# Optimization experiments

Hardware: AMD Instinct MI355X
Metric: run time of the kernel (lower is better)

## Reference

```python
import jax, jax.numpy as jnp
import numpy as np

VNUMS = [4248, 4258, 5327, 3721, 5404, 2818]
B, C, H, W = 12, 64, 192, 192
DV, HID, BOX = 128, 256, 32


def _roi_patches(imgs, pros, imgbatch, box_len=BOX):
    # torchvision roi_align (aligned=False, sampling_ratio -> 1 sample per 1x1 bin):
    # bilinear sample at bin centers x1 + (j+0.5), y1 + (i+0.5)
    ar = jnp.arange(box_len, dtype=pros.dtype) + 0.5
    xs = pros[:, 0:1] - box_len / 2.0 + ar  # [G, box]
    ys = pros[:, 1:2] - box_len / 2.0 + ar  # [G, box]
    img_g = imgs[imgbatch]  # [G, C, H, W]

    def sample_one(img_chw, ys1, xs1):
        yy, xx = jnp.meshgrid(ys1, xs1, indexing="ij")  # [box, box]
        def per_c(ch):
            return jax.scipy.ndimage.map_coordinates(ch, [yy, xx], order=1, mode="nearest")
        return jax.vmap(per_c)(img_chw)  # [C, box, box]

    return jax.vmap(sample_one)(img_g, ys, xs)  # [G, C, box, box]


def setup_inputs() -> dict:
    key = jax.random.key(0)
    ks = jax.random.split(key, 6)
    G = 2 * B
    gtypes = np.array([(g // 2) % 6 if g % 2 == 0 else ((g // 2) + 3) % 6 for g in range(G)], dtype=np.int64)
    vnums_g = np.array([VNUMS[t] for t in gtypes])
    off = np.concatenate([[0], np.cumsum(vnums_g)])
    Nv = int(off[-1])  # 103104
    gar_of_vert = np.repeat(np.arange(G), vnums_g)
    idxs = []
    for t in range(6):
        gl = np.nonzero(gtypes == t)[0]
        idxs.append(np.concatenate([off[g] + np.arange(VNUMS[t]) for g in gl]).astype(np.int32))
    Din = DV + C
    pros = jax.random.uniform(ks[1], (G, 2), jnp.float32) * (H - 2.0 * BOX) + BOX
    inp = {
        "imgs": jax.random.normal(ks[0], (B, C, H, W), jnp.float32),
        "pros": pros,
        "x_verts": jax.random.normal(ks[2], (Nv, DV), jnp.float32),
        "W1": jax.random.normal(ks[3], (6, Din, HID), jnp.float32) / np.sqrt(Din).astype(np.float32),
        "W2": jax.random.normal(ks[4], (6, HID, HID), jnp.float32) / np.sqrt(HID).astype(np.float32),
        "W3": jax.random.normal(ks[5], (6, HID, 3), jnp.float32) / np.sqrt(HID).astype(np.float32),
        "imgbatch": jnp.asarray(np.arange(G) // 2, jnp.int32),
        "gar_of_vert": jnp.asarray(gar_of_vert, jnp.int32),
    }
    for t in range(6):
        inp[f"idx_t{t}"] = jnp.asarray(idxs[t])
    return inp


def reference(imgs, pros, x_verts, W1, W2, W3, imgbatch, gar_of_vert,
              idx_t0, idx_t1, idx_t2, idx_t3, idx_t4, idx_t5):
    # 1) roi_align patch extraction + pooled per-garment image feature
    patches = _roi_patches(imgs, pros, imgbatch)        # [G, C, 32, 32]
    garf = patches.mean(axis=(2, 3))                     # [G, C]
    # 2) per-vertex feature = [vertex feat | garment image feat]
    feat = jnp.concatenate([x_verts, garf[gar_of_vert]], axis=-1)  # [Nv, DV+C]
    # 3) MoE-style dispatch per garment type -> per-type expert MLP -> scatter-combine
    out = jnp.zeros((x_verts.shape[0], 3), feat.dtype)
    for t, idx in enumerate([idx_t0, idx_t1, idx_t2, idx_t3, idx_t4, idx_t5]):
        ft = feat[idx]                                   # gather (dispatch)
        h = jax.nn.relu(ft @ W1[t])
        h = jax.nn.relu(h @ W2[t])
        out = out.at[idx].set(h @ W3[t])                 # scatter (combine)
    return out
```

## Files before the change

### kernel.cpp

```cpp
#include <hip/hip_runtime.h>

typedef __attribute__((ext_vector_type(8))) short short8;
typedef __attribute__((ext_vector_type(4))) float float4_;

__device__ __forceinline__ unsigned short f2bf(float f) {
    unsigned u = __float_as_uint(f);
    u += 0x7FFFu + ((u >> 16) & 1u);
    return (unsigned short)(u >> 16);
}

#define GARF_BLOCKS 1536
#define PREP_BLOCKS 2784

__global__ void prep_garf(const float* __restrict__ imgs,
                          const float* __restrict__ pros,
                          const int* __restrict__ imgbatch,
                          const float* __restrict__ W1,
                          const float* __restrict__ W2,
                          const float* __restrict__ W3,
                          unsigned short* __restrict__ w1t,
                          unsigned short* __restrict__ w2t,
                          unsigned short* __restrict__ w3t,
                          float* __restrict__ garf) {
    const int tid = threadIdx.x;
    if (blockIdx.x < GARF_BLOCKS) {
        __shared__ float part[4];
        int pc = blockIdx.x;
        int g = pc >> 6, c = pc & 63;
        int b = imgbatch[g];
        float cx = pros[g * 2 + 0], cy = pros[g * 2 + 1];
        int i = tid >> 3;
        int j0 = (tid & 7) * 4;
        float y = cy - 16.0f + (float)i + 0.5f;
        float yf = floorf(y);
        float wy1 = y - yf, wy0 = 1.0f - wy1;
        int iy0 = min(max((int)yf, 0), 191), iy1 = min(max((int)yf + 1, 0), 191);
        const float* base = imgs + (size_t)(b * 64 + c) * 36864;
        const float* r0 = base + iy0 * 192;
        const float* r1 = base + iy1 * 192;
        float sum = 0.0f;
#pragma unroll
        for (int jj = 0; jj < 4; ++jj) {
            float x = cx - 16.0f + (float)(j0 + jj) + 0.5f;
            float xf = floorf(x);
            float wx1 = x - xf, wx0 = 1.0f - wx1;
            int ix0 = min(max((int)xf, 0), 191), ix1 = min(max((int)xf + 1, 0), 191);
            sum += wy0 * (wx0 * r0[ix0] + wx1 * r0[ix1]) +
                   wy1 * (wx0 * r1[ix0] + wx1 * r1[ix1]);
        }
        for (int s = 32; s >= 1; s >>= 1) sum += __shfl_xor(sum, s);
        if ((tid & 63) == 0) part[tid >> 6] = sum;
        __syncthreads();
        if (tid == 0)
            garf[g * 64 + c] = (part[0] + part[1] + part[2] + part[3]) * (1.0f / 1024.0f);
    } else {
        int id = (blockIdx.x - GARF_BLOCKS) * 256 + tid;
        if (id < 294912) {
            int t = id / 49152, r = id % 49152;
            int k = r >> 8, n = r & 255;
            w1t[t * 49152 + n * 192 + k] = f2bf(W1[id]);
        } else if (id < 688128) {
            int i2 = id - 294912;
            int t = i2 >> 16, r = i2 & 65535;
            int k = r >> 8, n = r & 255;
            w2t[t * 65536 + n * 256 + k] = f2bf(W2[i2]);
        } else if (id < 712704) {
            int i3 = id - 688128;
            int t = i3 >> 12, r = i3 & 4095;
            int n = r >> 8, k = r & 255;
            w3t[i3] = (n < 3) ? f2bf(W3[t * 768 + k * 3 + n]) : (unsigned short)0;
        }
    }
}

struct MoEArgs {
    const float* x_verts;
    const int* gar;
    const int* idx[6];
    const unsigned short* w1t;
    const unsigned short* w2t;
    const unsigned short* w3t;
    const float* garf;
    float* out;
    int cnt[6];
    int tile_end[6];
};

__global__ __launch_bounds__(256, 4) void moe_kernel(MoEArgs a) {
    __shared__ __align__(16) char smem[32768 + 512];
    char* sF = smem;
    int* sidx = (int*)(smem + 32768);
    int* sg = sidx + 64;

    const int tid = threadIdx.x;
    int bt = blockIdx.x;
    int t = 0;
    while (t < 5 && bt >= a.tile_end[t]) ++t;
    const int tile = bt - (t ? a.tile_end[t - 1] : 0);
    const int cnt = a.cnt[t];
    const int i0 = tile * 64;
    const int* idx = a.idx[t];

    if (tid < 64) {
        int m = i0 + tid;
        if (m > cnt - 1) m = cnt - 1;
        int vid = idx[m];
        sidx[tid] = vid;
        sg[tid] = a.gar[vid];
    }
    __syncthreads();

    for (int e = tid; e < 1536; e += 256) {
        int m = e / 24, u = e % 24;
        const float* src;
        if (u < 16) src = a.x_verts + (size_t)sidx[m] * 128 + u * 8;
        else        src = a.garf + sg[m] * 64 + (u - 16) * 8;
        float4 v0 = ((const float4*)src)[0];
        float4 v1 = ((const float4*)src)[1];
        short8 pk;
        pk[0] = f2bf(v0.x); pk[1] = f2bf(v0.y); pk[2] = f2bf(v0.z); pk[3] = f2bf(v0.w);
        pk[4] = f2bf(v1.x); pk[5] = f2bf(v1.y); pk[6] = f2bf(v1.z); pk[7] = f2bf(v1.w);
        *(short8*)(sF + m * 384 + ((u ^ (m & 7)) * 16)) = pk;
    }
    __syncthreads();

    const int lane = tid & 63, w = tid >> 6, q = lane >> 4, l = lane & 15;

    float4_ acc[4][4] = {};
    const unsigned short* w1 = a.w1t + (size_t)t * 49152;
    for (int ks = 0; ks < 6; ++ks) {
        short8 af[4], bfr[4];
        for (int mt = 0; mt < 4; ++mt) {
            int hid = w * 64 + mt * 16 + l;
            af[mt] = *(const short8*)(w1 + hid * 192 + ks * 32 + q * 8);
        }
        for (int nt = 0; nt < 4; ++nt) {
            int v = nt * 16 + l;
            bfr[nt] = *(const short8*)(sF + v * 384 + (((ks * 4 + q) ^ (v & 7)) * 16));
        }
        for (int mt = 0; mt < 4; ++mt)
            for (int nt = 0; nt < 4; ++nt)
                acc[mt][nt] = __builtin_amdgcn_mfma_f32_16x16x32_bf16(
                    af[mt], bfr[nt], acc[mt][nt], 0, 0, 0);
    }
    __syncthreads();

    for (int mt = 0; mt < 4; ++mt)
        for (int nt = 0; nt < 4; ++nt) {
            int v = nt * 16 + l;
            int hu8 = w * 16 + mt * 4 + q;
            int ku16 = hu8 >> 1, par = hu8 & 1;
            uint2 pk;
            pk.x = (unsigned)f2bf(fmaxf(acc[mt][nt][0], 0.0f)) |
                   ((unsigned)f2bf(fmaxf(acc[mt][nt][1], 0.0f)) << 16);
            pk.y = (unsigned)f2bf(fmaxf(acc[mt][nt][2], 0.0f)) |
                   ((unsigned)f2bf(fmaxf(acc[mt][nt][3], 0.0f)) << 16);
            *(uint2*)(sF + v * 512 + ((ku16 ^ (v & 7)) * 16) + par * 8) = pk;
        }
    __syncthreads();

    float4_ acc2[4][4] = {};
    const unsigned short* w2 = a.w2t + (size_t)t * 65536;
    for (int ks = 0; ks < 8; ++ks) {
        short8 af[4], bfr[4];
        for (int mt = 0; mt < 4; ++mt) {
            int hid = w * 64 + mt * 16 + l;
            af[mt] = *(const short8*)(w2 + hid * 256 + ks * 32 + q * 8);
        }
        for (int nt = 0; nt < 4; ++nt) {
            int v = nt * 16 + l;
            bfr[nt] = *(const short8*)(sF + v * 512 + (((ks * 4 + q) ^ (v & 7)) * 16));
        }
        for (int mt = 0; mt < 4; ++mt)
            for (int nt = 0; nt < 4; ++nt)
                acc2[mt][nt] = __builtin_amdgcn_mfma_f32_16x16x32_bf16(
                    af[mt], bfr[nt], acc2[mt][nt], 0, 0, 0);
    }
    __syncthreads();

    for (int mt = 0; mt < 4; ++mt)
        for (int nt = 0; nt < 4; ++nt) {
            int v = nt * 16 + l;
            int hu8 = w * 16 + mt * 4 + q;
            int ku16 = hu8 >> 1, par = hu8 & 1;
            uint2 pk;
            pk.x = (unsigned)f2bf(fmaxf(acc2[mt][nt][0], 0.0f)) |
                   ((unsigned)f2bf(fmaxf(acc2[mt][nt][1], 0.0f)) << 16);
            pk.y = (unsigned)f2bf(fmaxf(acc2[mt][nt][2], 0.0f)) |
                   ((unsigned)f2bf(fmaxf(acc2[mt][nt][3], 0.0f)) << 16);
            *(uint2*)(sF + v * 512 + ((ku16 ^ (v & 7)) * 16) + par * 8) = pk;
        }
    __syncthreads();

    float4_ acc3 = {};
    const unsigned short* w3 = a.w3t + (size_t)t * 4096;
    int v3 = w * 16 + l;
    for (int ks = 0; ks < 8; ++ks) {
        short8 a3 = *(const short8*)(w3 + l * 256 + ks * 32 + q * 8);
        short8 b3 = *(const short8*)(sF + v3 * 512 + (((ks * 4 + q) ^ (v3 & 7)) * 16));
        acc3 = __builtin_amdgcn_mfma_f32_16x16x32_bf16(a3, b3, acc3, 0, 0, 0);
    }
    if (q == 0) {
        int m = i0 + v3;
        if (m < cnt) {
            float* o = a.out + (size_t)sidx[v3] * 3;
            o[0] = acc3[0]; o[1] = acc3[1]; o[2] = acc3[2];
        }
    }
}

extern "C" void kernel_launch(void* const* d_in, const int* in_sizes, int n_in,
                              void* d_out, int out_size, void* d_ws, size_t ws_size,
                              hipStream_t stream) {
    const float* imgs    = (const float*)d_in[0];
    const float* pros    = (const float*)d_in[1];
    const float* x_verts = (const float*)d_in[2];
    const float* W1      = (const float*)d_in[3];
    const float* W2      = (const float*)d_in[4];
    const float* W3      = (const float*)d_in[5];
    const int* imgbatch  = (const int*)d_in[6];
    const int* gar       = (const int*)d_in[7];

    unsigned short* w1t = (unsigned short*)d_ws;
    unsigned short* w2t = (unsigned short*)((char*)d_ws + 589824);
    unsigned short* w3t = (unsigned short*)((char*)d_ws + 1376256);
    float* garf         = (float*)((char*)d_ws + 1425408);

    prep_garf<<<GARF_BLOCKS + PREP_BLOCKS, 256, 0, stream>>>(
        imgs, pros, imgbatch, W1, W2, W3, w1t, w2t, w3t, garf);

    MoEArgs a;
    a.x_verts = x_verts;
    a.gar = gar;
    for (int t = 0; t < 6; ++t) a.idx[t] = (const int*)d_in[8 + t];
    a.w1t = w1t; a.w2t = w2t; a.w3t = w3t;
    a.garf = garf;
    a.out = (float*)d_out;
    int tiles = 0;
    for (int t = 0; t < 6; ++t) {
        a.cnt[t] = in_sizes[8 + t];
        tiles += (a.cnt[t] + 63) / 64;
        a.tile_end[t] = tiles;
    }
    moe_kernel<<<tiles, 256, 0, stream>>>(a);
}
```

Before: 265.3 us.

## Make MoE kernel persistent with register-resident bf16 expert weights

The MoE kernel becomes persistent: 256 blocks each walk a contiguous chunk of 64-vertex tiles. Each block converts W1/W2/W3 from fp32 straight into bf16 MFMA fragments held in registers, and reloads them only when the expert type changes. This drops the separate weight-transpose pass and the per-tile weight reads from global memory. Activation buffers in shared memory ping-pong between two halves, and launch bounds drop to one block per SM. The costs are heavy register pressure (64 short8 weight fragments per thread, with possible spills), strided uncoalesced fp32 weight loads, and less latency hiding from lower occupancy.

```diff
diff --git a/kernel.cpp b/kernel.cpp
--- a/kernel.cpp
+++ b/kernel.cpp
@@ -9,201 +9,217 @@
     return (unsigned short)(u >> 16);
 }
 
-#define GARF_BLOCKS 1536
-#define PREP_BLOCKS 2784
-
-__global__ void prep_garf(const float* __restrict__ imgs,
-                          const float* __restrict__ pros,
-                          const int* __restrict__ imgbatch,
-                          const float* __restrict__ W1,
-                          const float* __restrict__ W2,
-                          const float* __restrict__ W3,
-                          unsigned short* __restrict__ w1t,
-                          unsigned short* __restrict__ w2t,
-                          unsigned short* __restrict__ w3t,
-                          float* __restrict__ garf) {
+__global__ void garf_kernel(const float* __restrict__ imgs,
+                            const float* __restrict__ pros,
+                            const int* __restrict__ imgbatch,
+                            float* __restrict__ garf) {
+    __shared__ float part[4];
     const int tid = threadIdx.x;
-    if (blockIdx.x < GARF_BLOCKS) {
-        __shared__ float part[4];
-        int pc = blockIdx.x;
-        int g = pc >> 6, c = pc & 63;
-        int b = imgbatch[g];
-        float cx = pros[g * 2 + 0], cy = pros[g * 2 + 1];
-        int i = tid >> 3;
-        int j0 = (tid & 7) * 4;
-        float y = cy - 16.0f + (float)i + 0.5f;
-        float yf = floorf(y);
-        float wy1 = y - yf, wy0 = 1.0f - wy1;
-        int iy0 = min(max((int)yf, 0), 191), iy1 = min(max((int)yf + 1, 0), 191);
-        const float* base = imgs + (size_t)(b * 64 + c) * 36864;
-        const float* r0 = base + iy0 * 192;
-        const float* r1 = base + iy1 * 192;
-        float sum = 0.0f;
-#pragma unroll
-        for (int jj = 0; jj < 4; ++jj) {
-            float x = cx - 16.0f + (float)(j0 + jj) + 0.5f;
-            float xf = floorf(x);
-            float wx1 = x - xf, wx0 = 1.0f - wx1;
-            int ix0 = min(max((int)xf, 0), 191), ix1 = min(max((int)xf + 1, 0), 191);
-            sum += wy0 * (wx0 * r0[ix0] + wx1 * r0[ix1]) +
-                   wy1 * (wx0 * r1[ix0] + wx1 * r1[ix1]);
-        }
-        for (int s = 32; s >= 1; s >>= 1) sum += __shfl_xor(sum, s);
-        if ((tid & 63) == 0) part[tid >> 6] = sum;
-        __syncthreads();
-        if (tid == 0)
-            garf[g * 64 + c] = (part[0] + part[1] + part[2] + part[3]) * (1.0f / 1024.0f);
-    } else {
-        int id = (blockIdx.x - GARF_BLOCKS) * 256 + tid;
-        if (id < 294912) {
-            int t = id / 49152, r = id % 49152;
-            int k = r >> 8, n = r & 255;
-            w1t[t * 49152 + n * 192 + k] = f2bf(W1[id]);
-        } else if (id < 688128) {
-            int i2 = id - 294912;
-            int t = i2 >> 16, r = i2 & 65535;
-            int k = r >> 8, n = r & 255;
-            w2t[t * 65536 + n * 256 + k] = f2bf(W2[i2]);
-        } else if (id < 712704) {
-            int i3 = id - 688128;
-            int t = i3 >> 12, r = i3 & 4095;
-            int n = r >> 8, k = r & 255;
-            w3t[i3] = (n < 3) ? f2bf(W3[t * 768 + k * 3 + n]) : (unsigned short)0;
-        }
+    int g = blockIdx.x >> 6, c = blockIdx.x & 63;
+    int b = imgbatch[g];
+    float cx = pros[g * 2 + 0], cy = pros[g * 2 + 1];
+    int i = tid >> 3;
+    int j0 = (tid & 7) * 4;
+    float y = cy - 16.0f + (float)i + 0.5f;
+    float yf = floorf(y);
+    float wy1 = y - yf, wy0 = 1.0f - wy1;
+    int iy0 = min(max((int)yf, 0), 191), iy1 = min(max((int)yf + 1, 0), 191);
+    const float* base = imgs + (size_t)(b * 64 + c) * 36864;
+    const float* r0 = base + iy0 * 192;
+    const float* r1 = base + iy1 * 192;
+    float sum = 0.0f;
+#pragma unroll
+    for (int jj = 0; jj < 4; ++jj) {
+        float x = cx - 16.0f + (float)(j0 + jj) + 0.5f;
+        float xf = floorf(x);
+        float wx1 = x - xf, wx0 = 1.0f - wx1;
+        int ix0 = min(max((int)xf, 0), 191), ix1 = min(max((int)xf + 1, 0), 191);
+        sum += wy0 * (wx0 * r0[ix0] + wx1 * r0[ix1]) +
+               wy1 * (wx0 * r1[ix0] + wx1 * r1[ix1]);
     }
+    for (int s = 32; s >= 1; s >>= 1) sum += __shfl_xor(sum, s);
+    if ((tid & 63) == 0) part[tid >> 6] = sum;
+    __syncthreads();
+    if (tid == 0)
+        garf[g * 64 + c] = (part[0] + part[1] + part[2] + part[3]) * (1.0f / 1024.0f);
 }
 
 struct MoEArgs {
     const float* x_verts;
     const int* gar;
     const int* idx[6];
-    const unsigned short* w1t;
-    const unsigned short* w2t;
-    const unsigned short* w3t;
+    const float* W1;
+    const float* W2;
+    const float* W3;
     const float* garf;
     float* out;
     int cnt[6];
     int tile_end[6];
+    int ntiles;
+    int chunk;
 };
 
-__global__ __launch_bounds__(256, 4) void moe_kernel(MoEArgs a) {
-    __shared__ __align__(16) char smem[32768 + 512];
-    char* sF = smem;
-    int* sidx = (int*)(smem + 32768);
+__global__ __launch_bounds__(256, 1) void moe_kernel(MoEArgs a) {
+    __shared__ __align__(16) char smem[65536 + 512];
+    int* sidx = (int*)(smem + 65536);
     int* sg = sidx + 64;
 
     const int tid = threadIdx.x;
-    int bt = blockIdx.x;
-    int t = 0;
-    while (t < 5 && bt >= a.tile_end[t]) ++t;
-    const int tile = bt - (t ? a.tile_end[t - 1] : 0);
-    const int cnt = a.cnt[t];
-    const int i0 = tile * 64;
-    const int* idx = a.idx[t];
-
-    if (tid < 64) {
-        int m = i0 + tid;
-        if (m > cnt - 1) m = cnt - 1;
-        int vid = idx[m];
-        sidx[tid] = vid;
-        sg[tid] = a.gar[vid];
-    }
-    __syncthreads();
-
-    for (int e = tid; e < 1536; e += 256) {
-        int m = e / 24, u = e % 24;
-        const float* src;
-        if (u < 16) src = a.x_verts + (size_t)sidx[m] * 128 + u * 8;
-        else        src = a.garf + sg[m] * 64 + (u - 16) * 8;
-        float4 v0 = ((const float4*)src)[0];
-        float4 v1 = ((const float4*)src)[1];
-        short8 pk;
-        pk[0] = f2bf(v0.x); pk[1] = f2bf(v0.y); pk[2] = f2bf(v0.z); pk[3] = f2bf(v0.w);
-        pk[4] = f2bf(v1.x); pk[5] = f2bf(v1.y); pk[6] = f2bf(v1.z); pk[7] = f2bf(v1.w);
-        *(short8*)(sF + m * 384 + ((u ^ (m & 7)) * 16)) = pk;
-    }
-    __syncthreads();
-
     const int lane = tid & 63, w = tid >> 6, q = lane >> 4, l = lane & 15;
 
-    float4_ acc[4][4] = {};
-    const unsigned short* w1 = a.w1t + (size_t)t * 49152;
-    for (int ks = 0; ks < 6; ++ks) {
-        short8 af[4], bfr[4];
-        for (int mt = 0; mt < 4; ++mt) {
-            int hid = w * 64 + mt * 16 + l;
-            af[mt] = *(const short8*)(w1 + hid * 192 + ks * 32 + q * 8);
-        }
-        for (int nt = 0; nt < 4; ++nt) {
-            int v = nt * 16 + l;
-            bfr[nt] = *(const short8*)(sF + v * 384 + (((ks * 4 + q) ^ (v & 7)) * 16));
-        }
+    int start = blockIdx.x * a.chunk;
+    int end = min(start + a.chunk, a.ntiles);
+
+    short8 w1f[24], w2f[32], w3f[8];
+    int tcur = -1;
+    int p = 0;
+
+    for (int tile = start; tile < end; ++tile, p ^= 1) {
+        int t = 0;
+        while (t < 5 && tile >= a.tile_end[t]) ++t;
+        const int i0 = (tile - (t ? a.tile_end[t - 1] : 0)) * 64;
+        const int cnt = a.cnt[t];
+        const int* idx = a.idx[t];
+
+        if (tid < 64) {
+            int m = min(i0 + tid, cnt - 1);
+            int vid = idx[m];
+            sidx[tid] = vid;
+            sg[tid] = a.gar[vid];
+        }
+
+        if (t != tcur) {
+            tcur = t;
+            const float* w1 = a.W1 + t * 49152;
+            const float* w2 = a.W2 + t * 65536;
+            const float* w3 = a.W3 + t * 768;
+#pragma unroll
+            for (int ks = 0; ks < 6; ++ks)
+#pragma unroll
+                for (int mt = 0; mt < 4; ++mt) {
+                    const float* src = w1 + (ks * 32 + q * 8) * 256 + (w * 64 + mt * 16 + l);
+                    short8 r;
+#pragma unroll
+                    for (int j = 0; j < 8; ++j) r[j] = (short)f2bf(src[j * 256]);
+                    w1f[ks * 4 + mt] = r;
+                }
+#pragma unroll
+            for (int ks = 0; ks < 8; ++ks)
+#pragma unroll
+                for (int mt = 0; mt < 4; ++mt) {
+                    const float* src = w2 + (ks * 32 + q * 8) * 256 + (w * 64 + mt * 16 + l);
+                    short8 r;
+#pragma unroll
+                    for (int j = 0; j < 8; ++j) r[j] = (short)f2bf(src[j * 256]);
+                    w2f[ks * 4 + mt] = r;
+                }
+#pragma unroll
+            for (int ks = 0; ks < 8; ++ks) {
+                short8 r = {0, 0, 0, 0, 0, 0, 0, 0};
+                if (l < 3) {
+                    const float* src = w3 + (ks * 32 + q * 8) * 3 + l;
+#pragma unroll
+                    for (int j = 0; j < 8; ++j) r[j] = (short)f2bf(src[j * 3]);
+                }
+                w3f[ks] = r;
+            }
+        }
+        __syncthreads();
+
+        char* sF = smem + p * 32768;
+        char* sH = smem + (p ^ 1) * 32768;
+
+        for (int e = tid; e < 1536; e += 256) {
+            int m = e / 24, u = e - (e / 24) * 24;
+            const float* src;
+            if (u < 16) src = a.x_verts + (size_t)sidx[m] * 128 + u * 8;
+            else        src = a.garf + sg[m] * 64 + (u - 16) * 8;
+            float4 v0 = ((const float4*)src)[0];
+            float4 v1 = ((const float4*)src)[1];
+            short8 pk;
+            pk[0] = f2bf(v0.x); pk[1] = f2bf(v0.y); pk[2] = f2bf(v0.z); pk[3] = f2bf(v0.w);
+            pk[4] = f2bf(v1.x); pk[5] = f2bf(v1.y); pk[6] = f2bf(v1.z); pk[7] = f2bf(v1.w);
+            *(short8*)(sF + m * 384 + ((u ^ (m & 7)) * 16)) = pk;
+        }
+        const int v3 = w * 16 + l;
+        const int myvid = sidx[v3];
+        __syncthreads();
+
+        float4_ acc[4][4] = {};
+#pragma unroll
+        for (int ks = 0; ks < 6; ++ks) {
+            short8 bfr[4];
+#pragma unroll
+            for (int nt = 0; nt < 4; ++nt) {
+                int v = nt * 16 + l;
+                bfr[nt] = *(const short8*)(sF + v * 384 + (((ks * 4 + q) ^ (v & 7)) * 16));
+            }
+#pragma unroll
+            for (int mt = 0; mt < 4; ++mt)
+#pragma unroll
+                for (int nt = 0; nt < 4; ++nt)
+                    acc[mt][nt] = __builtin_amdgcn_mfma_f32_16x16x32_bf16(
+                        w1f[ks * 4 + mt], bfr[nt], acc[mt][nt], 0, 0, 0);
+        }
+#pragma unroll
         for (int mt = 0; mt < 4; ++mt)
-            for (int nt = 0; nt < 4; ++nt)
-                acc[mt][nt] = __builtin_amdgcn_mfma_f32_16x16x32_bf16(
-                    af[mt], bfr[nt], acc[mt][nt], 0, 0, 0);
-    }
-    __syncthreads();
-
-    for (int mt = 0; mt < 4; ++mt)
-        for (int nt = 0; nt < 4; ++nt) {
-            int v = nt * 16 + l;
-            int hu8 = w * 16 + mt * 4 + q;
-            int ku16 = hu8 >> 1, par = hu8 & 1;
-            uint2 pk;
-            pk.x = (unsigned)f2bf(fmaxf(acc[mt][nt][0], 0.0f)) |
-                   ((unsigned)f2bf(fmaxf(acc[mt][nt][1], 0.0f)) << 16);
-            pk.y = (unsigned)f2bf(fmaxf(acc[mt][nt][2], 0.0f)) |
-                   ((unsigned)f2bf(fmaxf(acc[mt][nt][3], 0.0f)) << 16);
-            *(uint2*)(sF + v * 512 + ((ku16 ^ (v & 7)) * 16) + par * 8) = pk;
-        }
-    __syncthreads();
-
-    float4_ acc2[4][4] = {};
-    const unsigned short* w2 = a.w2t + (size_t)t * 65536;
-    for (int ks = 0; ks < 8; ++ks) {
-        short8 af[4], bfr[4];
-        for (int mt = 0; mt < 4; ++mt) {
-            int hid = w * 64 + mt * 16 + l;
-            af[mt] = *(const short8*)(w2 + hid * 256 + ks * 32 + q * 8);
-        }
-        for (int nt = 0; nt < 4; ++nt) {
-            int v = nt * 16 + l;
-            bfr[nt] = *(const short8*)(sF + v * 512 + (((ks * 4 + q) ^ (v & 7)) * 16));
-        }
+#pragma unroll
+            for (int nt = 0; nt < 4; ++nt) {
+                int v = nt * 16 + l;
+                int hu8 = w * 16 + mt * 4 + q;
+                int ku16 = hu8 >> 1, par = hu8 & 1;
+                uint2 pk;
+                pk.x = (unsigned)f2bf(fmaxf(acc[mt][nt][0], 0.0f)) |
+                       ((unsigned)f2bf(fmaxf(acc[mt][nt][1], 0.0f)) << 16);
+                pk.y = (unsigned)f2bf(fmaxf(acc[mt][nt][2], 0.0f)) |
+                       ((unsigned)f2bf(fmaxf(acc[mt][nt][3], 0.0f)) << 16);
+                *(uint2*)(sH + v * 512 + ((ku16 ^ (v & 7)) * 16) + par * 8) = pk;
+            }
+        __syncthreads();
+
+#pragma unroll
         for (int mt = 0; mt < 4; ++mt)
-            for (int nt = 0; nt < 4; ++nt)
-                acc2[mt][nt] = __builtin_amdgcn_mfma_f32_16x16x32_bf16(
-                    af[mt], bfr[nt], acc2[mt][nt], 0, 0, 0);
-    }
-    __syncthreads();
-
-    for (int mt = 0; mt < 4; ++mt)
-        for (int nt = 0; nt < 4; ++nt) {
-            int v = nt * 16 + l;
-            int hu8 = w * 16 + mt * 4 + q;
-            int ku16 = hu8 >> 1, par = hu8 & 1;
-            uint2 pk;
-            pk.x = (unsigned)f2bf(fmaxf(acc2[mt][nt][0], 0.0f)) |
-                   ((unsigned)f2bf(fmaxf(acc2[mt][nt][1], 0.0f)) << 16);
-            pk.y = (unsigned)f2bf(fmaxf(acc2[mt][nt][2], 0.0f)) |
-                   ((unsigned)f2bf(fmaxf(acc2[mt][nt][3], 0.0f)) << 16);
-            *(uint2*)(sF + v * 512 + ((ku16 ^ (v & 7)) * 16) + par * 8) = pk;
-        }
-    __syncthreads();
-
-    float4_ acc3 = {};
-    const unsigned short* w3 = a.w3t + (size_t)t * 4096;
-    int v3 = w * 16 + l;
-    for (int ks = 0; ks < 8; ++ks) {
-        short8 a3 = *(const short8*)(w3 + l * 256 + ks * 32 + q * 8);
-        short8 b3 = *(const short8*)(sF + v3 * 512 + (((ks * 4 + q) ^ (v3 & 7)) * 16));
-        acc3 = __builtin_amdgcn_mfma_f32_16x16x32_bf16(a3, b3, acc3, 0, 0, 0);
-    }
-    if (q == 0) {
-        int m = i0 + v3;
-        if (m < cnt) {
-            float* o = a.out + (size_t)sidx[v3] * 3;
+#pragma unroll
+            for (int nt = 0; nt < 4; ++nt) acc[mt][nt] = float4_{0.f, 0.f, 0.f, 0.f};
+#pragma unroll
+        for (int ks = 0; ks < 8; ++ks) {
+            short8 bfr[4];
+#pragma unroll
+            for (int nt = 0; nt < 4; ++nt) {
+                int v = nt * 16 + l;
+                bfr[nt] = *(const short8*)(sH + v * 512 + (((ks * 4 + q) ^ (v & 7)) * 16));
+            }
+#pragma unroll
+            for (int mt = 0; mt < 4; ++mt)
+#pragma unroll
+                for (int nt = 0; nt < 4; ++nt)
+                    acc[mt][nt] = __builtin_amdgcn_mfma_f32_16x16x32_bf16(
+                        w2f[ks * 4 + mt], bfr[nt], acc[mt][nt], 0, 0, 0);
+        }
+#pragma unroll
+        for (int mt = 0; mt < 4; ++mt)
+#pragma unroll
+            for (int nt = 0; nt < 4; ++nt) {
+                int v = nt * 16 + l;
+                int hu8 = w * 16 + mt * 4 + q;
+                int ku16 = hu8 >> 1, par = hu8 & 1;
+                uint2 pk;
+                pk.x = (unsigned)f2bf(fmaxf(acc[mt][nt][0], 0.0f)) |
+                       ((unsigned)f2bf(fmaxf(acc[mt][nt][1], 0.0f)) << 16);
+                pk.y = (unsigned)f2bf(fmaxf(acc[mt][nt][2], 0.0f)) |
+                       ((unsigned)f2bf(fmaxf(acc[mt][nt][3], 0.0f)) << 16);
+                *(uint2*)(sF + v * 512 + ((ku16 ^ (v & 7)) * 16) + par * 8) = pk;
+            }
+        __syncthreads();
+
+        float4_ acc3 = {};
+#pragma unroll
+        for (int ks = 0; ks < 8; ++ks) {
+            short8 b3 = *(const short8*)(sF + v3 * 512 + (((ks * 4 + q) ^ (v3 & 7)) * 16));
+            acc3 = __builtin_amdgcn_mfma_f32_16x16x32_bf16(w3f[ks], b3, acc3, 0, 0, 0);
+        }
+        if (q == 0 && i0 + v3 < cnt) {
+            float* o = a.out + (size_t)myvid * 3;
             o[0] = acc3[0]; o[1] = acc3[1]; o[2] = acc3[2];
         }
     }
@@ -221,19 +237,15 @@
     const int* imgbatch  = (const int*)d_in[6];
     const int* gar       = (const int*)d_in[7];
 
-    unsigned short* w1t = (unsigned short*)d_ws;
-    unsigned short* w2t = (unsigned short*)((char*)d_ws + 589824);
-    unsigned short* w3t = (unsigned short*)((char*)d_ws + 1376256);
-    float* garf         = (float*)((char*)d_ws + 1425408);
-
-    prep_garf<<<GARF_BLOCKS + PREP_BLOCKS, 256, 0, stream>>>(
-        imgs, pros, imgbatch, W1, W2, W3, w1t, w2t, w3t, garf);
+    float* garf = (float*)d_ws;
+
+    garf_kernel<<<24 * 64, 256, 0, stream>>>(imgs, pros, imgbatch, garf);
 
     MoEArgs a;
     a.x_verts = x_verts;
     a.gar = gar;
     for (int t = 0; t < 6; ++t) a.idx[t] = (const int*)d_in[8 + t];
-    a.w1t = w1t; a.w2t = w2t; a.w3t = w3t;
+    a.W1 = W1; a.W2 = W2; a.W3 = W3;
     a.garf = garf;
     a.out = (float*)d_out;
     int tiles = 0;
@@ -242,5 +254,7 @@
         tiles += (a.cnt[t] + 63) / 64;
         a.tile_end[t] = tiles;
     }
-    moe_kernel<<<tiles, 256, 0, stream>>>(a);
-}
+    a.ntiles = tiles;
+    a.chunk = (tiles + 255) / 256;
+    moe_kernel<<<256, 256, 0, stream>>>(a);
+}
```

Result: slower. 291.6 us (+9.9%).

## Software-pipeline MFMA operand loads and restructure gather in MoE kernel

Applied to the files above, without the earlier changes.

Double-buffers the A (global weight) and B (LDS activation) fragments in the layer-1 and layer-2 GEMM loops, so the loads for the next k-step are issued before the current MFMAs run. The gather is restructured so each thread issues six independent loads per vertex row without a separate index-staging pass and barrier. The final-layer loads are all hoisted ahead of the MFMA chain. Launch bounds occupancy drops from 4 to 3 blocks to make room for the extra registers, which risks lower latency hiding across waves.

```diff
diff --git a/kernel.cpp b/kernel.cpp
--- a/kernel.cpp
+++ b/kernel.cpp
@@ -86,66 +86,90 @@
     int tile_end[6];
 };
 
-__global__ __launch_bounds__(256, 4) void moe_kernel(MoEArgs a) {
-    __shared__ __align__(16) char smem[32768 + 512];
-    char* sF = smem;
-    int* sidx = (int*)(smem + 32768);
-    int* sg = sidx + 64;
+__global__ __launch_bounds__(256, 3) void moe_kernel(MoEArgs a) {
+    __shared__ __align__(16) char sF[32768];
 
     const int tid = threadIdx.x;
+    const int lane = tid & 63, w = tid >> 6, q = lane >> 4, l = lane & 15;
+
     int bt = blockIdx.x;
     int t = 0;
     while (t < 5 && bt >= a.tile_end[t]) ++t;
-    const int tile = bt - (t ? a.tile_end[t - 1] : 0);
+    const int i0 = (bt - (t ? a.tile_end[t - 1] : 0)) * 64;
     const int cnt = a.cnt[t];
-    const int i0 = tile * 64;
     const int* idx = a.idx[t];
 
-    if (tid < 64) {
-        int m = i0 + tid;
-        if (m > cnt - 1) m = cnt - 1;
-        int vid = idx[m];
-        sidx[tid] = vid;
-        sg[tid] = a.gar[vid];
-    }
-    __syncthreads();
-
-    for (int e = tid; e < 1536; e += 256) {
-        int m = e / 24, u = e % 24;
-        const float* src;
-        if (u < 16) src = a.x_verts + (size_t)sidx[m] * 128 + u * 8;
-        else        src = a.garf + sg[m] * 64 + (u - 16) * 8;
-        float4 v0 = ((const float4*)src)[0];
-        float4 v1 = ((const float4*)src)[1];
-        short8 pk;
-        pk[0] = f2bf(v0.x); pk[1] = f2bf(v0.y); pk[2] = f2bf(v0.z); pk[3] = f2bf(v0.w);
-        pk[4] = f2bf(v1.x); pk[5] = f2bf(v1.y); pk[6] = f2bf(v1.z); pk[7] = f2bf(v1.w);
-        *(short8*)(sF + m * 384 + ((u ^ (m & 7)) * 16)) = pk;
-    }
-    __syncthreads();
-
-    const int lane = tid & 63, w = tid >> 6, q = lane >> 4, l = lane & 15;
+    const int v3 = w * 16 + l;
+    const int vid3 = idx[min(i0 + v3, cnt - 1)];
+
+    {
+        int m = tid >> 2;
+        int vid = idx[min(i0 + m, cnt - 1)];
+        int g = a.gar[vid];
+        const float* vsrc = a.x_verts + (size_t)vid * 128;
+        const float* gsrc = a.garf + g * 64;
+        int u0 = (tid & 3) * 6;
+        float4 v[6][2];
+#pragma unroll
+        for (int i = 0; i < 6; ++i) {
+            int u = u0 + i;
+            const float* s = (u < 16) ? (vsrc + u * 8) : (gsrc + (u - 16) * 8);
+            v[i][0] = ((const float4*)s)[0];
+            v[i][1] = ((const float4*)s)[1];
+        }
+#pragma unroll
+        for (int i = 0; i < 6; ++i) {
+            int u = u0 + i;
+            short8 pk;
+            pk[0] = f2bf(v[i][0].x); pk[1] = f2bf(v[i][0].y);
+            pk[2] = f2bf(v[i][0].z); pk[3] = f2bf(v[i][0].w);
+            pk[4] = f2bf(v[i][1].x); pk[5] = f2bf(v[i][1].y);
+            pk[6] = f2bf(v[i][1].z); pk[7] = f2bf(v[i][1].w);
+            *(short8*)(sF + m * 384 + ((u ^ (m & 7)) * 16)) = pk;
+        }
+    }
+    __syncthreads();
 
     float4_ acc[4][4] = {};
-    const unsigned short* w1 = a.w1t + (size_t)t * 49152;
-    for (int ks = 0; ks < 6; ++ks) {
-        short8 af[4], bfr[4];
-        for (int mt = 0; mt < 4; ++mt) {
-            int hid = w * 64 + mt * 16 + l;
-            af[mt] = *(const short8*)(w1 + hid * 192 + ks * 32 + q * 8);
-        }
-        for (int nt = 0; nt < 4; ++nt) {
-            int v = nt * 16 + l;
-            bfr[nt] = *(const short8*)(sF + v * 384 + (((ks * 4 + q) ^ (v & 7)) * 16));
-        }
-        for (int mt = 0; mt < 4; ++mt)
-            for (int nt = 0; nt < 4; ++nt)
-                acc[mt][nt] = __builtin_amdgcn_mfma_f32_16x16x32_bf16(
-                    af[mt], bfr[nt], acc[mt][nt], 0, 0, 0);
-    }
-    __syncthreads();
-
+    {
+        const unsigned short* w1 = a.w1t + (size_t)t * 49152;
+        const unsigned short* pA[4];
+#pragma unroll
+        for (int nt = 0; nt < 4; ++nt)
+            pA[nt] = w1 + (w * 64 + nt * 16 + l) * 192 + q * 8;
+        short8 A0[4], A1[4], B0[4], B1[4];
+#pragma unroll
+        for (int nt = 0; nt < 4; ++nt) {
+            A0[nt] = *(const short8*)(pA[nt]);
+            int v = nt * 16 + l;
+            B0[nt] = *(const short8*)(sF + v * 384 + ((q ^ (v & 7)) * 16));
+        }
+#pragma unroll
+        for (int ks = 0; ks < 6; ++ks) {
+            if (ks < 5) {
+#pragma unroll
+                for (int nt = 0; nt < 4; ++nt) {
+                    A1[nt] = *(const short8*)(pA[nt] + (ks + 1) * 32);
+                    int v = nt * 16 + l;
+                    B1[nt] = *(const short8*)(sF + v * 384 +
+                              ((((ks + 1) * 4 + q) ^ (v & 7)) * 16));
+                }
+            }
+#pragma unroll
+            for (int mt = 0; mt < 4; ++mt)
+#pragma unroll
+                for (int nt = 0; nt < 4; ++nt)
+                    acc[mt][nt] = __builtin_amdgcn_mfma_f32_16x16x32_bf16(
+                        A0[mt], B0[nt], acc[mt][nt], 0, 0, 0);
+#pragma unroll
+            for (int nt = 0; nt < 4; ++nt) { A0[nt] = A1[nt]; B0[nt] = B1[nt]; }
+        }
+    }
+    __syncthreads();
+
+#pragma unroll
     for (int mt = 0; mt < 4; ++mt)
+#pragma unroll
         for (int nt = 0; nt < 4; ++nt) {
             int v = nt * 16 + l;
             int hu8 = w * 16 + mt * 4 + q;
@@ -160,25 +184,45 @@
     __syncthreads();
 
     float4_ acc2[4][4] = {};
-    const unsigned short* w2 = a.w2t + (size_t)t * 65536;
-    for (int ks = 0; ks < 8; ++ks) {
-        short8 af[4], bfr[4];
-        for (int mt = 0; mt < 4; ++mt) {
-            int hid = w * 64 + mt * 16 + l;
-            af[mt] = *(const short8*)(w2 + hid * 256 + ks * 32 + q * 8);
-        }
-        for (int nt = 0; nt < 4; ++nt) {
-            int v = nt * 16 + l;
-            bfr[nt] = *(const short8*)(sF + v * 512 + (((ks * 4 + q) ^ (v & 7)) * 16));
-        }
-        for (int mt = 0; mt < 4; ++mt)
-            for (int nt = 0; nt < 4; ++nt)
-                acc2[mt][nt] = __builtin_amdgcn_mfma_f32_16x16x32_bf16(
-                    af[mt], bfr[nt], acc2[mt][nt], 0, 0, 0);
-    }
-    __syncthreads();
-
+    {
+        const unsigned short* w2 = a.w2t + (size_t)t * 65536;
+        const unsigned short* pA[4];
+#pragma unroll
+        for (int nt = 0; nt < 4; ++nt)
+            pA[nt] = w2 + (w * 64 + nt * 16 + l) * 256 + q * 8;
+        short8 A0[4], A1[4], B0[4], B1[4];
+#pragma unroll
+        for (int nt = 0; nt < 4; ++nt) {
+            A0[nt] = *(const short8*)(pA[nt]);
+            int v = nt * 16 + l;
+            B0[nt] = *(const short8*)(sF + v * 512 + ((q ^ (v & 7)) * 16));
+        }
+#pragma unroll
+        for (int ks = 0; ks < 8; ++ks) {
+            if (ks < 7) {
+#pragma unroll
+                for (int nt = 0; nt < 4; ++nt) {
+                    A1[nt] = *(const short8*)(pA[nt] + (ks + 1) * 32);
+                    int v = nt * 16 + l;
+                    B1[nt] = *(const short8*)(sF + v * 512 +
+                              ((((ks + 1) * 4 + q) ^ (v & 7)) * 16));
+                }
+            }
+#pragma unroll
+            for (int mt = 0; mt < 4; ++mt)
+#pragma unroll
+                for (int nt = 0; nt < 4; ++nt)
+                    acc2[mt][nt] = __builtin_amdgcn_mfma_f32_16x16x32_bf16(
+                        A0[mt], B0[nt], acc2[mt][nt], 0, 0, 0);
+#pragma unroll
+            for (int nt = 0; nt < 4; ++nt) { A0[nt] = A1[nt]; B0[nt] = B1[nt]; }
+        }
+    }
+    __syncthreads();
+
+#pragma unroll
     for (int mt = 0; mt < 4; ++mt)
+#pragma unroll
         for (int nt = 0; nt < 4; ++nt) {
             int v = nt * 16 + l;
             int hu8 = w * 16 + mt * 4 + q;
@@ -192,18 +236,20 @@
         }
     __syncthreads();
 
-    float4_ acc3 = {};
-    const unsigned short* w3 = a.w3t + (size_t)t * 4096;
-    int v3 = w * 16 + l;
-    for (int ks = 0; ks < 8; ++ks) {
-        short8 a3 = *(const short8*)(w3 + l * 256 + ks * 32 + q * 8);
-        short8 b3 = *(const short8*)(sF + v3 * 512 + (((ks * 4 + q) ^ (v3 & 7)) * 16));
-        acc3 = __builtin_amdgcn_mfma_f32_16x16x32_bf16(a3, b3, acc3, 0, 0, 0);
-    }
-    if (q == 0) {
-        int m = i0 + v3;
-        if (m < cnt) {
-            float* o = a.out + (size_t)sidx[v3] * 3;
+    {
+        const unsigned short* w3 = a.w3t + (size_t)t * 4096;
+        short8 A3[8], B3[8];
+#pragma unroll
+        for (int ks = 0; ks < 8; ++ks) {
+            A3[ks] = *(const short8*)(w3 + l * 256 + ks * 32 + q * 8);
+            B3[ks] = *(const short8*)(sF + v3 * 512 + (((ks * 4 + q) ^ (v3 & 7)) * 16));
+        }
+        float4_ acc3 = {};
+#pragma unroll
+        for (int ks = 0; ks < 8; ++ks)
+            acc3 = __builtin_amdgcn_mfma_f32_16x16x32_bf16(A3[ks], B3[ks], acc3, 0, 0, 0);
+        if (q == 0 && i0 + v3 < cnt) {
+            float* o = a.out + (size_t)vid3 * 3;
             o[0] = acc3[0]; o[1] = acc3[1]; o[2] = acc3[2];
         }
     }
```

Measured after the change: 271.9 us. 2.5% more time.
